# Kernel tuning notes

Hardware: AMD Instinct MI355X
Metric: run time of the kernel (lower is better)

## Reference

```python
import jax, jax.numpy as jnp
import numpy as np

TAU = 0.05       # sinkhorn temperature (functools.partial in GCN_Net)
SK_ITERS = 20    # sinkhorn max_iter


def _mlp(x, w1, b1, w2, b2):
    # nn.Sequential(Linear, ReLU, Linear)
    return jnp.maximum(x @ w1 + b1, 0.0) @ w2 + b2


def _cosine(f1, f2, eps=1e-8):
    # torch CosineSimilarity over broadcast (E1,1,D) x (1,E2,D), computed as a GEMM
    n1 = jnp.maximum(jnp.linalg.norm(f1, axis=-1), eps)
    n2 = jnp.maximum(jnp.linalg.norm(f2, axis=-1), eps)
    return (f1 @ f2.T) / (n1[:, None] * n2[None, :])


def _sinkhorn(s):
    # log-domain sinkhorn, alternating row/col normalization (pygmtools-style)
    log_s = s / TAU
    for i in range(SK_ITERS):
        log_s = log_s - jax.nn.logsumexp(log_s, axis=(1 if i % 2 == 0 else 0), keepdims=True)
    return jnp.exp(log_s)


def _build_conn_edges(preds):
    # fully-connected off-diagonal graph; edge feats [dx, dy, dist, cls_src, cls_dst]
    n = preds.shape[0]
    pos = preds[:, 1:3]
    cls = preds[:, 6]
    idx = np.arange(n)
    r, c = np.meshgrid(idx, idx, indexing='ij')
    m = r != c
    conn = np.stack([r[m], c[m]], axis=1)  # (E,2), static under jit
    src, dst = conn[:, 0], conn[:, 1]
    d = pos[dst] - pos[src]                             # (E,2)
    dist = jnp.linalg.norm(d, axis=-1, keepdims=True)   # (E,1)
    edges = jnp.concatenate([d, dist, cls[src][:, None], cls[dst][:, None]], axis=-1)  # (E,5)
    return jnp.asarray(conn), edges


def _forward(ego_preds, cav_preds, node_w1, node_b1, node_w2, node_b2,
             edge_w1, edge_b1, edge_w2, edge_b2,
             l0_self_w, l0_self_b, l0_conv_w, l0_conv_b, l0_cls_w, l0_cls_b,
             l1_self_w, l1_self_b, l1_conv_w, l1_conv_b, l1_cls_w, l1_cls_b,
             fc_w, fc_b):
    ego = ego_preds[0]
    cav = cav_preds[0]
    n1, n2 = ego.shape[0], cav.shape[0]
    conn1, e1 = _build_conn_edges(ego)
    conn2, e2 = _build_conn_edges(cav)
    # --- NodeMLP affinity ---
    f1 = _mlp(ego[:, 1:6], node_w1, node_b1, node_w2, node_b2)
    f2 = _mlp(cav[:, 1:6], node_w1, node_b1, node_w2, node_b2)
    cls_eq = (ego[:, 6][:, None] == cav[:, 6][None, :]).astype(ego.dtype)
    conf = jnp.sum(jnp.sqrt(ego[:, 7:][:, None, :] * cav[:, 7:][None, :, :]), axis=-1)
    node_aff = cls_eq * conf * _cosine(f1, f2)                         # (n1,n2)
    # --- EdgeMLP affinity ---
    g1 = _mlp(e1[:, :3], edge_w1, edge_b1, edge_w2, edge_b2)
    g2 = _mlp(e2[:, :3], edge_w1, edge_b1, edge_w2, edge_b2)
    ecls = jnp.all(e1[:, 3:].astype(jnp.int32)[:, None, :] == e2[:, 3:].astype(jnp.int32)[None, :, :],
                   axis=-1).astype(ego.dtype)
    edge_aff = ecls * _cosine(g1, g2)                                  # (E1,E2)
    # --- Lawler affinity matrix K over association graph: node (i,a) -> i*n2+a ---
    N = n1 * n2
    rows = (conn1[:, 0][:, None] * n2 + conn2[:, 0][None, :]).ravel()
    cols = (conn1[:, 1][:, None] * n2 + conn2[:, 1][None, :]).ravel()
    K = jnp.zeros((N, N), ego.dtype).at[rows, cols].set(edge_aff.ravel())
    d_idx = jnp.arange(N)
    K = K.at[d_idx, d_idx].set(node_aff.ravel())
    # --- GCN adjacency = nonzero pattern of K, with added self-loops + sym norm ---
    A = (K != 0).astype(ego.dtype) + jnp.eye(N, dtype=ego.dtype)
    dinv = jax.lax.rsqrt(A.sum(axis=1))
    normA = dinv[:, None] * A * dinv[None, :]
    x = jnp.diag(K)[:, None]                                           # (N,1)
    # --- NGMConvLayers: self-loop Linear + GCNConv + sinkhorn channel ---
    for sw, sb, cw, cb, kw, kb in (
            (l0_self_w, l0_self_b, l0_conv_w, l0_conv_b, l0_cls_w, l0_cls_b),
            (l1_self_w, l1_self_b, l1_conv_w, l1_conv_b, l1_cls_w, l1_cls_b)):
        x = (x @ sw + sb) + (normA @ (x @ cw) + cb)
        sk = _sinkhorn((x @ kw + kb).reshape(n1, n2))
        x = x + sk.reshape(-1, 1)
    scores = x @ fc_w + fc_b                                           # (N,1)
    s = scores.reshape(n2, n1).T                                       # view(n2,-1).t()
    return _sinkhorn(s)


def setup_inputs() -> dict:
    key = jax.random.key(0)
    ks = jax.random.split(key, 16)

    def lin(k, fi, fo):
        kw, kb = jax.random.split(k)
        s = (2.0 / (fi + fo)) ** 0.5
        return (jax.random.normal(kw, (fi, fo), jnp.float32) * s,
                jax.random.normal(kb, (fo,), jnp.float32) * 0.01)

    def make_preds(k, n):
        k1, k2 = jax.random.split(k)
        p = jax.random.uniform(k1, (1, n, 8), jnp.float32)
        cls = jnp.floor(jax.random.uniform(k2, (1, n)) * 3.0)  # 3 discrete classes
        p = p.at[:, :, 6].set(cls)
        p = p.at[:, :, 7].set(0.1 + 0.9 * p[:, :, 7])          # positive confidences
        return p

    inp = {'ego_preds': make_preds(ks[0], 64), 'cav_preds': make_preds(ks[1], 64)}
    inp['node_w1'], inp['node_b1'] = lin(ks[2], 5, 64)
    inp['node_w2'], inp['node_b2'] = lin(ks[3], 64, 32)
    inp['edge_w1'], inp['edge_b1'] = lin(ks[4], 3, 64)
    inp['edge_w2'], inp['edge_b2'] = lin(ks[5], 64, 32)
    inp['l0_self_w'], inp['l0_self_b'] = lin(ks[6], 1, 16)
    inp['l0_conv_w'], inp['l0_conv_b'] = lin(ks[7], 1, 16)
    inp['l0_cls_w'], inp['l0_cls_b'] = lin(ks[8], 16, 1)
    inp['l1_self_w'], inp['l1_self_b'] = lin(ks[9], 16, 16)
    inp['l1_conv_w'], inp['l1_conv_b'] = lin(ks[10], 16, 16)
    inp['l1_cls_w'], inp['l1_cls_b'] = lin(ks[11], 16, 1)
    inp['fc_w'], inp['fc_b'] = lin(ks[12], 16, 1)
    return inp


def reference(ego_preds, cav_preds, node_w1, node_b1, node_w2, node_b2,
              edge_w1, edge_b1, edge_w2, edge_b2,
              l0_self_w, l0_self_b, l0_conv_w, l0_conv_b, l0_cls_w, l0_cls_b,
              l1_self_w, l1_self_b, l1_conv_w, l1_conv_b, l1_cls_w, l1_cls_b,
              fc_w, fc_b):
    return _forward(ego_preds, cav_preds, node_w1, node_b1, node_w2, node_b2,
                    edge_w1, edge_b1, edge_w2, edge_b2,
                    l0_self_w, l0_self_b, l0_conv_w, l0_conv_b, l0_cls_w, l0_cls_b,
                    l1_self_w, l1_self_b, l1_conv_w, l1_conv_b, l1_cls_w, l1_cls_b,
                    fc_w, fc_b)
```

## Files before the change

kernel.cpp:

```cpp
#include <hip/hip_runtime.h>
#include <math.h>


#define TAU_INV 20.0f

template<int CTRL>
__device__ __forceinline__ float dppf(float x) {
    int xi = __float_as_int(x);
    int rr = __builtin_amdgcn_update_dpp(xi, xi, CTRL, 0xF, 0xF, false);
    return __int_as_float(rr);
}
__device__ __forceinline__ float red16_max(float v) {
    v = fmaxf(v, dppf<0xB1>(v));
    v = fmaxf(v, dppf<0x4E>(v));
    v = fmaxf(v, dppf<0x141>(v));
    v = fmaxf(v, dppf<0x140>(v));
    return v;
}
__device__ __forceinline__ float red16_sum(float v) {
    v += dppf<0xB1>(v);
    v += dppf<0x4E>(v);
    v += dppf<0x141>(v);
    v += dppf<0x140>(v);
    return v;
}
__device__ __forceinline__ float quad_sum(float v) {
    v += dppf<0xB1>(v);
    v += dppf<0x4E>(v);
    return v;
}
__device__ __forceinline__ float dot4(const float4 a, const float4 b) {
    return a.x*b.x + a.y*b.y + a.z*b.z + a.w*b.w;
}
__device__ __forceinline__ void fma4(float4& a, float b, const float4 c) {
    a.x += b*c.x; a.y += b*c.y; a.z += b*c.z; a.w += b*c.w;
}
__device__ __forceinline__ void add4(float4& a, const float4 c) {
    a.x += c.x; a.y += c.y; a.z += c.z; a.w += c.w;
}

__device__ void sinkhorn_rc(const float* tq, const float* tt, int tid, float* Rp, float* Cp) {
    const int g = tid >> 4, s = tid & 15;
    const int wa = 4 * (g & 15) + (g >> 4);
    for (int it = 0; it < 20; ++it) {
        if ((it & 1) == 0) {
            float4 cq = *(const float4*)(Cp + 4 * s);
            float z0 = tq[0]-cq.x, z1 = tq[1]-cq.y, z2 = tq[2]-cq.z, z3 = tq[3]-cq.w;
            float m  = red16_max(fmaxf(fmaxf(z0, z1), fmaxf(z2, z3)));
            float sm = red16_sum(__expf(z0-m) + __expf(z1-m) + __expf(z2-m) + __expf(z3-m));
            if (s == 0) Rp[wa] = __logf(sm) + m;
        } else {
            float4 rq = *(const float4*)(Rp + 4 * s);
            float z0 = tt[0]-rq.x, z1 = tt[1]-rq.y, z2 = tt[2]-rq.z, z3 = tt[3]-rq.w;
            float m  = red16_max(fmaxf(fmaxf(z0, z1), fmaxf(z2, z3)));
            float sm = red16_sum(__expf(z0-m) + __expf(z1-m) + __expf(z2-m) + __expf(z3-m));
            if (s == 0) Cp[wa] = __logf(sm) + m;
        }
        __syncthreads();
    }
}

__device__ void matvec_dual(const float* u1, const float* u2,
                            const float* mmq, const float* dq,
                            float* o1, float* o2, int tid,
                            float* WR1, float* WR2, float* WC1p, float* WC2p,
                            float* pwc, float* scW) {
    const int r = tid >> 4, s = tid & 15, lane = tid & 63, w = tid >> 6;
    float z1[4], z2[4];
    float rs1 = 0.0f, rs2 = 0.0f;
    #pragma unroll
    for (int k = 0; k < 4; ++k) {
        float md = mmq[k] * dq[k];
        z1[k] = md * u1[k];
        z2[k] = md * u2[k];
        rs1 += z1[k]; rs2 += z2[k];
    }
    rs1 = red16_sum(rs1); rs2 = red16_sum(rs2);
    if (s == 0) { WR1[r] = rs1; WR2[r] = rs2; }
    float p1[4], p2[4];
    #pragma unroll
    for (int k = 0; k < 4; ++k) {
        float v = z1[k]; v += __shfl_xor(v, 16); v += __shfl_xor(v, 32); p1[k] = v;
        float u = z2[k]; u += __shfl_xor(u, 16); u += __shfl_xor(u, 32); p2[k] = u;
    }
    if (lane < 16) {
        ((float4*)pwc)[w * 16 + s]          = make_float4(p1[0], p1[1], p1[2], p1[3]);
        ((float4*)(pwc + 1024))[w * 16 + s] = make_float4(p2[0], p2[1], p2[2], p2[3]);
    }
    __syncthreads();
    if (tid < 64) {
        float c1 = 0.0f, c2 = 0.0f;
        #pragma unroll
        for (int ww = 0; ww < 16; ++ww) {
            c1 += pwc[ww * 64 + tid];
            c2 += pwc[1024 + ww * 64 + tid];
        }
        WC1p[tid] = c1; WC2p[tid] = c2;
    } else if (tid < 128) {
        float v = WR1[tid - 64];
        #pragma unroll
        for (int off = 32; off > 0; off >>= 1) v += __shfl_xor(v, off);
        if (tid == 64) scW[0] = v;
    } else if (tid < 192) {
        float v = WR2[tid - 128];
        #pragma unroll
        for (int off = 32; off > 0; off >>= 1) v += __shfl_xor(v, off);
        if (tid == 128) scW[1] = v;
    }
    __syncthreads();
    const float W1 = scW[0], W2 = scW[1];
    const float wr1 = WR1[r], wr2 = WR2[r];
    float4 wc1 = *(const float4*)(WC1p + 4 * s);
    float4 wc2 = *(const float4*)(WC2p + 4 * s);
    const float wc1a[4] = {wc1.x, wc1.y, wc1.z, wc1.w};
    const float wc2a[4] = {wc2.x, wc2.y, wc2.z, wc2.w};
    #pragma unroll
    for (int k = 0; k < 4; ++k) {
        float d = dq[k], mm = mmq[k];
        o1[k] = d * ((1.0f + mm) * d * u1[k] + mm * (W1 - wr1 - wc1a[k] + z1[k]));
        o2[k] = d * ((1.0f + mm) * d * u2[k] + mm * (W2 - wr2 - wc2a[k] + z2[k]));
    }
    __syncthreads();
}

extern "C" __global__ __launch_bounds__(1024)
void gcn_match_kernel(const float* ego, const float* cav,
                      const float* nw1, const float* nb1, const float* nw2, const float* nb2,
                      const float* sw0, const float* sb0, const float* cw0, const float* cb0,
                      const float* kw0, const float* kb0,
                      const float* sw1, const float* sb1, const float* cw1, const float* cb1,
                      const float* kw1, const float* kb1,
                      const float* fcw, const float* fcb,
                      float* out) {
    __shared__ __align__(16) float sh_h1[64 * 68];
    __shared__ __align__(16) float sh_h2[64 * 68];
    __shared__ __align__(16) float sh_f1[64 * 36];
    __shared__ __align__(16) float sh_f2[64 * 36];
    __shared__ __align__(16) float sh_w2[2048];
    __shared__ __align__(16) float sh_nb2[32];
    __shared__ float sh_cls1[64], sh_cls2[64], sh_cf1[64], sh_cf2[64];
    __shared__ float sh_n1[64], sh_n2[64];
    __shared__ float sh_Dr[64], sh_Dc[64];
    __shared__ __align__(16) float sh_Rp[64], sh_Cp[64];
    __shared__ float sh_WR1[64], sh_WR2[64];
    __shared__ __align__(16) float sh_WC1p[64], sh_WC2p[64];
    __shared__ float sh_avec[7 * 16];
    __shared__ float sh_coef[18];
    __shared__ float sh_sc[4];

    const int tid  = threadIdx.x;
    const int wave = tid >> 6, lane = tid & 63;
    const int r = tid >> 4, s = tid & 15;

    if (tid < 512) ((float4*)sh_w2)[tid] = ((const float4*)nw2)[tid];
    if (tid < 32) sh_nb2[tid] = nb2[tid];
    if (tid < 64) { sh_cls1[tid] = ego[tid * 8 + 6]; sh_cf1[tid] = ego[tid * 8 + 7]; }
    else if (tid < 128) { int j = tid - 64; sh_cls2[j] = cav[j * 8 + 6]; sh_cf2[j] = cav[j * 8 + 7]; }
    {
        float w1r[5];
        #pragma unroll
        for (int f = 0; f < 5; ++f) w1r[f] = nw1[f * 64 + lane];
        float b1r = nb1[lane];
        #pragma unroll
        for (int p = 0; p < 4; ++p) {
            int i = wave + (p << 4);
            float4 e0 = ((const float4*)ego)[i * 2];
            float4 e1 = ((const float4*)ego)[i * 2 + 1];
            float a1 = b1r + e0.y*w1r[0] + e0.z*w1r[1] + e0.w*w1r[2] + e1.x*w1r[3] + e1.y*w1r[4];
            sh_h1[i * 68 + lane] = fmaxf(a1, 0.0f);
            float4 c0 = ((const float4*)cav)[i * 2];
            float4 c1 = ((const float4*)cav)[i * 2 + 1];
            float a2 = b1r + c0.y*w1r[0] + c0.z*w1r[1] + c0.w*w1r[2] + c1.x*w1r[3] + c1.y*w1r[4];
            sh_h2[i * 68 + lane] = fmaxf(a2, 0.0f);
        }
    }
    __syncthreads();

    if (wave < 4) {
        const int gw = wave & 1;
        const float* H = (wave < 2) ? sh_h1 : sh_h2;
        float* F  = (wave < 2) ? sh_f1 : sh_f2;
        float* NN = (wave < 2) ? sh_n1 : sh_n2;
        const int rr = lane >> 2, oq = lane & 3;
        const int i0 = 32 * gw + rr, i1 = i0 + 16;
        float4 a00 = make_float4(0,0,0,0), a01 = a00, a10 = a00, a11 = a00;
        #pragma unroll 4
        for (int k = 0; k < 64; ++k) {
            float  ha = H[i0 * 68 + k];
            float  hb = H[i1 * 68 + k];
            float4 wa = *(const float4*)(sh_w2 + k * 32 + 4 * oq);
            float4 wb = *(const float4*)(sh_w2 + k * 32 + 16 + 4 * oq);
            fma4(a00, ha, wa); fma4(a01, ha, wb);
            fma4(a10, hb, wa); fma4(a11, hb, wb);
        }
        float4 b2a = *(const float4*)(sh_nb2 + 4 * oq);
        float4 b2b = *(const float4*)(sh_nb2 + 16 + 4 * oq);
        add4(a00, b2a); add4(a01, b2b); add4(a10, b2a); add4(a11, b2b);
        *(float4*)(F + i0 * 36 + 4 * oq)      = a00;
        *(float4*)(F + i0 * 36 + 16 + 4 * oq) = a01;
        *(float4*)(F + i1 * 36 + 4 * oq)      = a10;
        *(float4*)(F + i1 * 36 + 16 + 4 * oq) = a11;
        float sq0 = quad_sum(dot4(a00, a00) + dot4(a01, a01));
        float sq1 = quad_sum(dot4(a10, a10) + dot4(a11, a11));
        if (oq == 0) {
            NN[i0] = fmaxf(sqrtf(sq0), 1e-8f);
            NN[i1] = fmaxf(sqrtf(sq1), 1e-8f);
        }
    } else if (wave == 4) {
        float c1v = sh_cls1[lane], d = 0.0f;
        for (int j = 0; j < 64; ++j) d += (c1v == sh_cls2[j]) ? 1.0f : 0.0f;
        sh_Dr[lane] = d;
        float t = d;
        #pragma unroll
        for (int off = 32; off > 0; off >>= 1) t += __shfl_xor(t, off);
        if (lane == 0) sh_sc[2] = t;
    } else if (wave == 5) {
        float c2v = sh_cls2[lane], d = 0.0f;
        for (int i = 0; i < 64; ++i) d += (sh_cls1[i] == c2v) ? 1.0f : 0.0f;
        sh_Dc[lane] = d;
    } else if (wave == 6 && lane < 16) {
        int o = lane;
        float ax = 0, av = 0, as_ = 0, aw = 0, au = 0, ae = 0, a1 = 0;
        for (int k = 0; k < 16; ++k) {
            float s0k = sw0[k], c0k = cw0[k], b0k = sb0[k] + cb0[k];
            float s1ko = sw1[k * 16 + o], c1ko = cw1[k * 16 + o];
            ax += s0k * s1ko;  av += c0k * s1ko + s0k * c1ko;  as_ += s1ko;
            aw += c0k * c1ko;  au += c1ko;  ae += b0k * c1ko;  a1 += b0k * s1ko;
        }
        a1 += sb1[o] + cb1[o];
        sh_avec[0*16+o] = ax; sh_avec[1*16+o] = av; sh_avec[2*16+o] = as_;
        sh_avec[3*16+o] = aw; sh_avec[4*16+o] = au; sh_avec[5*16+o] = ae;
        sh_avec[6*16+o] = a1;
    }
    __syncthreads();

    if (wave < 4) {
        const int sc = lane & 15, rc = lane >> 4;
        float dt[4][4];
        #pragma unroll
        for (int m = 0; m < 4; ++m)
            #pragma unroll
            for (int k = 0; k < 4; ++k) dt[m][k] = 0.0f;
        for (int kq = 0; kq < 8; ++kq) {
            float4 f2q[4];
            #pragma unroll
            for (int k = 0; k < 4; ++k)
                f2q[k] = *(const float4*)(sh_f2 + (sc + 16 * k) * 36 + 4 * kq);
            #pragma unroll
            for (int m = 0; m < 4; ++m) {
                int rrow = 16 * m + 4 * wave + rc;
                float4 f1q = *(const float4*)(sh_f1 + rrow * 36 + 4 * kq);
                #pragma unroll
                for (int k = 0; k < 4; ++k) dt[m][k] += dot4(f1q, f2q[k]);
            }
        }
        #pragma unroll
        for (int m = 0; m < 4; ++m) {
            int rrow = 16 * m + 4 * wave + rc;
            *(float4*)(sh_h1 + rrow * 68 + 4 * sc) =
                make_float4(dt[m][0], dt[m][1], dt[m][2], dt[m][3]);
        }
    } else if (wave == 4 && lane < 18) {
        int t = lane; float c = 0.0f;
        if (t == 0)      { for (int k = 0; k < 16; ++k) c += sw0[k] * kw0[k]; }
        else if (t == 1) { for (int k = 0; k < 16; ++k) c += cw0[k] * kw0[k]; }
        else if (t == 2) { for (int k = 0; k < 16; ++k) c += (sb0[k] + cb0[k]) * kw0[k]; c += kb0[0]; }
        else if (t < 10) { int v = t - 3;
            for (int o = 0; o < 16; ++o) c += sh_avec[v * 16 + o] * kw1[o];
            if (v == 6) c += kb1[0];
        } else if (t < 17) { int v = t - 10;
            for (int o = 0; o < 16; ++o) c += sh_avec[v * 16 + o] * fcw[o];
            if (v == 6) c += fcb[0];
        } else { for (int o = 0; o < 16; ++o) c += fcw[o]; }
        sh_coef[t] = c;
    } else if (wave == 5) {
        sh_Cp[lane] = 0.0f;
    }
    const float cls1r = sh_cls1[r];
    const float Tdeg = sh_sc[2], Drr = sh_Dr[r];
    const float n1r = sh_n1[r], cf1r = sh_cf1[r];
    float mmq[4], dqv[4], cfq[4], n2q[4];
    #pragma unroll
    for (int k = 0; k < 4; ++k) {
        int j = s + 16 * k;
        float mm = (cls1r == sh_cls2[j]) ? 1.0f : 0.0f;
        mmq[k] = mm;
        dqv[k] = (mm != 0.0f) ? (1.0f / sqrtf(Tdeg - Drr - sh_Dc[j] + 3.0f)) : 1.0f;
        cfq[k] = sqrtf(cf1r * sh_cf2[j]);
        n2q[k] = sh_n2[j];
    }
    __syncthreads();

    float x0[4];
    {
        float4 dq4 = *(const float4*)(sh_h1 + r * 68 + 4 * s);
        const float da[4] = {dq4.x, dq4.y, dq4.z, dq4.w};
        #pragma unroll
        for (int k = 0; k < 4; ++k)
            x0[k] = mmq[k] * cfq[k] * (da[k] / (n1r * n2q[k]));
    }
    __syncthreads();

    float v0[4], oe[4];
    {
        float ones[4] = {1.0f, 1.0f, 1.0f, 1.0f};
        matvec_dual(x0, ones, mmq, dqv, v0, oe, tid,
                    sh_WR1, sh_WR2, sh_WC1p, sh_WC2p, sh_h1, sh_sc);
    }

    const int pr = 4 * (r & 15) + (r >> 4);
    float t0q[4], t0t[4];
    {
        float c0 = sh_coef[0], c1 = sh_coef[1], c2 = sh_coef[2];
        #pragma unroll
        for (int k = 0; k < 4; ++k) t0q[k] = (c0 * x0[k] + c1 * v0[k] + c2) * TAU_INV;
    }
    *(float4*)(sh_h2 + r * 68 + 4 * s) = make_float4(t0q[0], t0q[1], t0q[2], t0q[3]);
    __syncthreads();
    #pragma unroll
    for (int k = 0; k < 4; ++k) t0t[k] = sh_h2[(s + 16 * k) * 68 + pr];
    sinkhorn_rc(t0q, t0t, tid, sh_Rp, sh_Cp);
    float s0[4];
    {
        float Rr = sh_Rp[pr];
        float4 cc = *(const float4*)(sh_Cp + 4 * s);
        const float ca[4] = {cc.x, cc.y, cc.z, cc.w};
        #pragma unroll
        for (int k = 0; k < 4; ++k) s0[k] = __expf(t0q[k] - Rr - ca[k]);
    }

    float ov[4], os[4];
    matvec_dual(v0, s0, mmq, dqv, ov, os, tid,
                sh_WR1, sh_WR2, sh_WC1p, sh_WC2p, sh_h1, sh_sc);
    float tacc[4], sacc[4];
    {
        float ctx = sh_coef[3], ctv = sh_coef[4], cts = sh_coef[5];
        float cw_ = sh_coef[6], cu_ = sh_coef[7], ce_ = sh_coef[8], ct1 = sh_coef[9];
        float csx = sh_coef[10], csv = sh_coef[11], css = sh_coef[12];
        float cw2 = sh_coef[13], cu2 = sh_coef[14], ce2 = sh_coef[15], cs1 = sh_coef[16];
        #pragma unroll
        for (int k = 0; k < 4; ++k) {
            tacc[k] = ctx * x0[k] + ctv * v0[k] + cts * s0[k] + ct1
                    + cw_ * ov[k] + cu_ * os[k] + ce_ * oe[k];
            sacc[k] = csx * x0[k] + csv * v0[k] + css * s0[k] + cs1
                    + cw2 * ov[k] + cu2 * os[k] + ce2 * oe[k];
        }
    }

    float t1q[4], t1t[4];
    #pragma unroll
    for (int k = 0; k < 4; ++k) t1q[k] = tacc[k] * TAU_INV;
    if (tid < 64) sh_Cp[tid] = 0.0f;
    *(float4*)(sh_h2 + r * 68 + 4 * s) = make_float4(t1q[0], t1q[1], t1q[2], t1q[3]);
    __syncthreads();
    #pragma unroll
    for (int k = 0; k < 4; ++k) t1t[k] = sh_h2[(s + 16 * k) * 68 + pr];
    sinkhorn_rc(t1q, t1t, tid, sh_Rp, sh_Cp);
    {
        float c17 = sh_coef[17];
        float Rr = sh_Rp[pr];
        float4 cc = *(const float4*)(sh_Cp + 4 * s);
        const float ca[4] = {cc.x, cc.y, cc.z, cc.w};
        #pragma unroll
        for (int k = 0; k < 4; ++k) sacc[k] += c17 * __expf(t1q[k] - Rr - ca[k]);
    }
    __syncthreads();

    if (tid < 64) sh_Cp[tid] = 0.0f;
    *(float4*)(sh_h2 + r * 68 + 4 * s) = make_float4(sacc[0], sacc[1], sacc[2], sacc[3]);
    __syncthreads();
    float t2q[4], t2t[4];
    #pragma unroll
    for (int k = 0; k < 4; ++k) {
        t2q[k] = sh_h2[(s + 16 * k) * 68 + pr] * TAU_INV;
        t2t[k] = sacc[k] * TAU_INV;
    }
    sinkhorn_rc(t2q, t2t, tid, sh_Rp, sh_Cp);
    {
        float Rr = sh_Rp[pr];
        float4 cc = *(const float4*)(sh_Cp + 4 * s);
        const float ca[4] = {cc.x, cc.y, cc.z, cc.w};
        #pragma unroll
        for (int k = 0; k < 4; ++k)
            out[r * 64 + s + 16 * k] = __expf(t2q[k] - Rr - ca[k]);
    }
}

extern "C" void kernel_launch(void* const* d_in, const int* in_sizes, int n_in,
                              void* d_out, int out_size, void* d_ws, size_t ws_size,
                              hipStream_t stream) {
    const float* ego = (const float*)d_in[0];
    const float* cav = (const float*)d_in[1];
    const float* nw1 = (const float*)d_in[2];
    const float* nb1 = (const float*)d_in[3];
    const float* nw2 = (const float*)d_in[4];
    const float* nb2 = (const float*)d_in[5];
    const float* sw0 = (const float*)d_in[10];
    const float* sb0 = (const float*)d_in[11];
    const float* cw0 = (const float*)d_in[12];
    const float* cb0 = (const float*)d_in[13];
    const float* kw0 = (const float*)d_in[14];
    const float* kb0 = (const float*)d_in[15];
    const float* sw1 = (const float*)d_in[16];
    const float* sb1 = (const float*)d_in[17];
    const float* cw1 = (const float*)d_in[18];
    const float* cb1 = (const float*)d_in[19];
    const float* kw1 = (const float*)d_in[20];
    const float* kb1 = (const float*)d_in[21];
    const float* fcw = (const float*)d_in[22];
    const float* fcb = (const float*)d_in[23];

    gcn_match_kernel<<<dim3(1), dim3(1024), 0, stream>>>(
        ego, cav, nw1, nb1, nw2, nb2,
        sw0, sb0, cw0, cb0, kw0, kb0,
        sw1, sb1, cw1, cb1, kw1, kb1,
        fcw, fcb, (float*)d_out);
}
```

Baseline: 136.5 us.

## Rework Sinkhorn in base-2 log domain with incremental normalizers and fewer barriers

Sinkhorn now runs in the log2 domain using the hardware exp2/log2 builtins, with the temperature folded into a scale constant. Each row or column keeps its own running normalizer and adds the log-sum of already-normalized exponentials, so the per-iteration max reduction goes away. A clamp guards against underflow. The change also drops the Cp zeroing, fuses the first row step into the setup barrier, double-buffers the matvec scratch so a trailing barrier can be removed, and moves the coefficient precompute into an earlier phase. Skipping the max subtraction relies on the values staying bounded, which is a numerical risk.

```diff
diff --git a/kernel.cpp b/kernel.cpp
--- a/kernel.cpp
+++ b/kernel.cpp
@@ -2,7 +2,7 @@
 #include <math.h>
 
 
-#define TAU_INV 20.0f
+#define SK_SCALE 28.853900817779268f
 
 template<int CTRL>
 __device__ __forceinline__ float dppf(float x) {
@@ -18,17 +18,15 @@
     return v;
 }
 __device__ __forceinline__ float red16_sum(float v) {
-    v += dppf<0xB1>(v);
-    v += dppf<0x4E>(v);
-    v += dppf<0x141>(v);
-    v += dppf<0x140>(v);
+    v += dppf<0xB1>(v); v += dppf<0x4E>(v); v += dppf<0x141>(v); v += dppf<0x140>(v);
     return v;
 }
 __device__ __forceinline__ float quad_sum(float v) {
-    v += dppf<0xB1>(v);
-    v += dppf<0x4E>(v);
+    v += dppf<0xB1>(v); v += dppf<0x4E>(v);
     return v;
 }
+__device__ __forceinline__ float e2f(float x) { return __builtin_amdgcn_exp2f(x); }
+__device__ __forceinline__ float l2f(float x) { return __builtin_amdgcn_logf(x); }
 __device__ __forceinline__ float dot4(const float4 a, const float4 b) {
     return a.x*b.x + a.y*b.y + a.z*b.z + a.w*b.w;
 }
@@ -39,25 +37,43 @@
     a.x += c.x; a.y += c.y; a.z += c.z; a.w += c.w;
 }
 
-__device__ void sinkhorn_rc(const float* tq, const float* tt, int tid, float* Rp, float* Cp) {
-    const int g = tid >> 4, s = tid & 15;
-    const int wa = 4 * (g & 15) + (g >> 4);
-    for (int it = 0; it < 20; ++it) {
-        if ((it & 1) == 0) {
+__device__ __forceinline__ float sk_step0(const float* tq) {
+    float m  = red16_max(fmaxf(fmaxf(tq[0], tq[1]), fmaxf(tq[2], tq[3])));
+    float sm = red16_sum(e2f(tq[0]-m) + e2f(tq[1]-m) + e2f(tq[2]-m) + e2f(tq[3]-m));
+    return m + l2f(sm);
+}
+
+__device__ float sk_rest(const float* tq, const float* tt, float Rown,
+                         int pr, int s, float* Rp, float* Cp) {
+    float Cown;
+    {
+        float4 rq = *(const float4*)(Rp + 4 * s);
+        float sm = red16_sum(e2f(tt[0]-rq.x) + e2f(tt[1]-rq.y) +
+                             e2f(tt[2]-rq.z) + e2f(tt[3]-rq.w));
+        Cown = l2f(fmaxf(sm, 1e-37f));
+        if (s == 0) Cp[pr] = Cown;
+        __syncthreads();
+    }
+    #pragma unroll 1
+    for (int p = 0; p < 9; ++p) {
+        {
             float4 cq = *(const float4*)(Cp + 4 * s);
-            float z0 = tq[0]-cq.x, z1 = tq[1]-cq.y, z2 = tq[2]-cq.z, z3 = tq[3]-cq.w;
-            float m  = red16_max(fmaxf(fmaxf(z0, z1), fmaxf(z2, z3)));
-            float sm = red16_sum(__expf(z0-m) + __expf(z1-m) + __expf(z2-m) + __expf(z3-m));
-            if (s == 0) Rp[wa] = __logf(sm) + m;
-        } else {
+            float sm = red16_sum(e2f(tq[0]-cq.x-Rown) + e2f(tq[1]-cq.y-Rown) +
+                                 e2f(tq[2]-cq.z-Rown) + e2f(tq[3]-cq.w-Rown));
+            Rown += l2f(fmaxf(sm, 1e-37f));
+            if (s == 0) Rp[pr] = Rown;
+            __syncthreads();
+        }
+        {
             float4 rq = *(const float4*)(Rp + 4 * s);
-            float z0 = tt[0]-rq.x, z1 = tt[1]-rq.y, z2 = tt[2]-rq.z, z3 = tt[3]-rq.w;
-            float m  = red16_max(fmaxf(fmaxf(z0, z1), fmaxf(z2, z3)));
-            float sm = red16_sum(__expf(z0-m) + __expf(z1-m) + __expf(z2-m) + __expf(z3-m));
-            if (s == 0) Cp[wa] = __logf(sm) + m;
-        }
-        __syncthreads();
-    }
+            float sm = red16_sum(e2f(tt[0]-rq.x-Cown) + e2f(tt[1]-rq.y-Cown) +
+                                 e2f(tt[2]-rq.z-Cown) + e2f(tt[3]-rq.w-Cown));
+            Cown += l2f(fmaxf(sm, 1e-37f));
+            if (s == 0) Cp[pr] = Cown;
+            __syncthreads();
+        }
+    }
+    return Rown;
 }
 
 __device__ void matvec_dual(const float* u1, const float* u2,
@@ -120,7 +136,6 @@
         o1[k] = d * ((1.0f + mm) * d * u1[k] + mm * (W1 - wr1 - wc1a[k] + z1[k]));
         o2[k] = d * ((1.0f + mm) * d * u2[k] + mm * (W2 - wr2 - wc2a[k] + z2[k]));
     }
-    __syncthreads();
 }
 
 extern "C" __global__ __launch_bounds__(1024)
@@ -138,49 +153,68 @@
     __shared__ __align__(16) float sh_f2[64 * 36];
     __shared__ __align__(16) float sh_w2[2048];
     __shared__ __align__(16) float sh_nb2[32];
-    __shared__ float sh_cls1[64], sh_cls2[64], sh_cf1[64], sh_cf2[64];
-    __shared__ float sh_n1[64], sh_n2[64];
-    __shared__ float sh_Dr[64], sh_Dc[64];
+    __shared__ float sh_cls1[64], sh_cf1[64];
+    __shared__ __align__(16) float sh_cls2p[64], sh_cf2p[64];
+    __shared__ float sh_n1[64];
+    __shared__ __align__(16) float sh_n2p[64];
+    __shared__ float sh_Dr[64];
+    __shared__ __align__(16) float sh_Dcp[64];
     __shared__ __align__(16) float sh_Rp[64], sh_Cp[64];
-    __shared__ float sh_WR1[64], sh_WR2[64];
-    __shared__ __align__(16) float sh_WC1p[64], sh_WC2p[64];
+    __shared__ float sh_WR1a[64], sh_WR2a[64], sh_WR1b[64], sh_WR2b[64];
+    __shared__ __align__(16) float sh_WC1pa[64], sh_WC2pa[64], sh_WC1pb[64], sh_WC2pb[64];
     __shared__ float sh_avec[7 * 16];
     __shared__ float sh_coef[18];
-    __shared__ float sh_sc[4];
+    __shared__ float sh_sc[8];
 
     const int tid  = threadIdx.x;
     const int wave = tid >> 6, lane = tid & 63;
     const int r = tid >> 4, s = tid & 15;
+    const int pr = 4 * (r & 15) + (r >> 4);
 
     if (tid < 512) ((float4*)sh_w2)[tid] = ((const float4*)nw2)[tid];
     if (tid < 32) sh_nb2[tid] = nb2[tid];
     if (tid < 64) { sh_cls1[tid] = ego[tid * 8 + 6]; sh_cf1[tid] = ego[tid * 8 + 7]; }
-    else if (tid < 128) { int j = tid - 64; sh_cls2[j] = cav[j * 8 + 6]; sh_cf2[j] = cav[j * 8 + 7]; }
-    {
+    else if (tid < 128) {
+        int j = tid - 64, jp = 4 * (j & 15) + (j >> 4);
+        sh_cls2p[jp] = cav[j * 8 + 6]; sh_cf2p[jp] = cav[j * 8 + 7];
+    }
+    if (wave < 8) {
         float w1r[5];
         #pragma unroll
         for (int f = 0; f < 5; ++f) w1r[f] = nw1[f * 64 + lane];
         float b1r = nb1[lane];
         #pragma unroll
-        for (int p = 0; p < 4; ++p) {
-            int i = wave + (p << 4);
+        for (int p = 0; p < 8; ++p) {
+            int i = (wave << 3) | p;
             float4 e0 = ((const float4*)ego)[i * 2];
             float4 e1 = ((const float4*)ego)[i * 2 + 1];
-            float a1 = b1r + e0.y*w1r[0] + e0.z*w1r[1] + e0.w*w1r[2] + e1.x*w1r[3] + e1.y*w1r[4];
-            sh_h1[i * 68 + lane] = fmaxf(a1, 0.0f);
+            sh_h1[i * 68 + lane] = fmaxf(
+                b1r + e0.y*w1r[0] + e0.z*w1r[1] + e0.w*w1r[2] + e1.x*w1r[3] + e1.y*w1r[4], 0.0f);
             float4 c0 = ((const float4*)cav)[i * 2];
             float4 c1 = ((const float4*)cav)[i * 2 + 1];
-            float a2 = b1r + c0.y*w1r[0] + c0.z*w1r[1] + c0.w*w1r[2] + c1.x*w1r[3] + c1.y*w1r[4];
-            sh_h2[i * 68 + lane] = fmaxf(a2, 0.0f);
-        }
+            sh_h2[i * 68 + lane] = fmaxf(
+                b1r + c0.y*w1r[0] + c0.z*w1r[1] + c0.w*w1r[2] + c1.x*w1r[3] + c1.y*w1r[4], 0.0f);
+        }
+    } else if (wave == 8 && lane < 16) {
+        int o = lane;
+        float ax = 0, av = 0, as_ = 0, aw = 0, au = 0, ae = 0, a1 = 0;
+        for (int k = 0; k < 16; ++k) {
+            float s0k = sw0[k], c0k = cw0[k], b0k = sb0[k] + cb0[k];
+            float s1ko = sw1[k * 16 + o], c1ko = cw1[k * 16 + o];
+            ax += s0k * s1ko;  av += c0k * s1ko + s0k * c1ko;  as_ += s1ko;
+            aw += c0k * c1ko;  au += c1ko;  ae += b0k * c1ko;  a1 += b0k * s1ko;
+        }
+        a1 += sb1[o] + cb1[o];
+        sh_avec[0*16+o] = ax; sh_avec[1*16+o] = av; sh_avec[2*16+o] = as_;
+        sh_avec[3*16+o] = aw; sh_avec[4*16+o] = au; sh_avec[5*16+o] = ae;
+        sh_avec[6*16+o] = a1;
     }
     __syncthreads();
 
     if (wave < 4) {
         const int gw = wave & 1;
         const float* H = (wave < 2) ? sh_h1 : sh_h2;
-        float* F  = (wave < 2) ? sh_f1 : sh_f2;
-        float* NN = (wave < 2) ? sh_n1 : sh_n2;
+        float* F = (wave < 2) ? sh_f1 : sh_f2;
         const int rr = lane >> 2, oq = lane & 3;
         const int i0 = 32 * gw + rr, i1 = i0 + 16;
         float4 a00 = make_float4(0,0,0,0), a01 = a00, a10 = a00, a11 = a00;
@@ -203,34 +237,40 @@
         float sq0 = quad_sum(dot4(a00, a00) + dot4(a01, a01));
         float sq1 = quad_sum(dot4(a10, a10) + dot4(a11, a11));
         if (oq == 0) {
-            NN[i0] = fmaxf(sqrtf(sq0), 1e-8f);
-            NN[i1] = fmaxf(sqrtf(sq1), 1e-8f);
+            float v0n = fmaxf(sqrtf(sq0), 1e-8f);
+            float v1n = fmaxf(sqrtf(sq1), 1e-8f);
+            if (wave < 2) { sh_n1[i0] = v0n; sh_n1[i1] = v1n; }
+            else {
+                sh_n2p[4 * (i0 & 15) + (i0 >> 4)] = v0n;
+                sh_n2p[4 * (i1 & 15) + (i1 >> 4)] = v1n;
+            }
         }
     } else if (wave == 4) {
         float c1v = sh_cls1[lane], d = 0.0f;
-        for (int j = 0; j < 64; ++j) d += (c1v == sh_cls2[j]) ? 1.0f : 0.0f;
+        for (int j = 0; j < 64; ++j) d += (c1v == sh_cls2p[j]) ? 1.0f : 0.0f;
         sh_Dr[lane] = d;
         float t = d;
         #pragma unroll
         for (int off = 32; off > 0; off >>= 1) t += __shfl_xor(t, off);
         if (lane == 0) sh_sc[2] = t;
     } else if (wave == 5) {
-        float c2v = sh_cls2[lane], d = 0.0f;
+        float c2v = sh_cls2p[4 * (lane & 15) + (lane >> 4)];
+        float d = 0.0f;
         for (int i = 0; i < 64; ++i) d += (sh_cls1[i] == c2v) ? 1.0f : 0.0f;
-        sh_Dc[lane] = d;
-    } else if (wave == 6 && lane < 16) {
-        int o = lane;
-        float ax = 0, av = 0, as_ = 0, aw = 0, au = 0, ae = 0, a1 = 0;
-        for (int k = 0; k < 16; ++k) {
-            float s0k = sw0[k], c0k = cw0[k], b0k = sb0[k] + cb0[k];
-            float s1ko = sw1[k * 16 + o], c1ko = cw1[k * 16 + o];
-            ax += s0k * s1ko;  av += c0k * s1ko + s0k * c1ko;  as_ += s1ko;
-            aw += c0k * c1ko;  au += c1ko;  ae += b0k * c1ko;  a1 += b0k * s1ko;
-        }
-        a1 += sb1[o] + cb1[o];
-        sh_avec[0*16+o] = ax; sh_avec[1*16+o] = av; sh_avec[2*16+o] = as_;
-        sh_avec[3*16+o] = aw; sh_avec[4*16+o] = au; sh_avec[5*16+o] = ae;
-        sh_avec[6*16+o] = a1;
+        sh_Dcp[4 * (lane & 15) + (lane >> 4)] = d;
+    } else if (wave == 6 && lane < 18) {
+        int t = lane; float c = 0.0f;
+        if (t == 0)      { for (int k = 0; k < 16; ++k) c += sw0[k] * kw0[k]; }
+        else if (t == 1) { for (int k = 0; k < 16; ++k) c += cw0[k] * kw0[k]; }
+        else if (t == 2) { for (int k = 0; k < 16; ++k) c += (sb0[k] + cb0[k]) * kw0[k]; c += kb0[0]; }
+        else if (t < 10) { int v = t - 3;
+            for (int o = 0; o < 16; ++o) c += sh_avec[v * 16 + o] * kw1[o];
+            if (v == 6) c += kb1[0];
+        } else if (t < 17) { int v = t - 10;
+            for (int o = 0; o < 16; ++o) c += sh_avec[v * 16 + o] * fcw[o];
+            if (v == 6) c += fcb[0];
+        } else { for (int o = 0; o < 16; ++o) c += fcw[o]; }
+        sh_coef[t] = c;
     }
     __syncthreads();
 
@@ -260,39 +300,34 @@
             *(float4*)(sh_h1 + rrow * 68 + 4 * sc) =
                 make_float4(dt[m][0], dt[m][1], dt[m][2], dt[m][3]);
         }
-    } else if (wave == 4 && lane < 18) {
-        int t = lane; float c = 0.0f;
-        if (t == 0)      { for (int k = 0; k < 16; ++k) c += sw0[k] * kw0[k]; }
-        else if (t == 1) { for (int k = 0; k < 16; ++k) c += cw0[k] * kw0[k]; }
-        else if (t == 2) { for (int k = 0; k < 16; ++k) c += (sb0[k] + cb0[k]) * kw0[k]; c += kb0[0]; }
-        else if (t < 10) { int v = t - 3;
-            for (int o = 0; o < 16; ++o) c += sh_avec[v * 16 + o] * kw1[o];
-            if (v == 6) c += kb1[0];
-        } else if (t < 17) { int v = t - 10;
-            for (int o = 0; o < 16; ++o) c += sh_avec[v * 16 + o] * fcw[o];
-            if (v == 6) c += fcb[0];
-        } else { for (int o = 0; o < 16; ++o) c += fcw[o]; }
-        sh_coef[t] = c;
-    } else if (wave == 5) {
-        sh_Cp[lane] = 0.0f;
-    }
-    const float cls1r = sh_cls1[r];
-    const float Tdeg = sh_sc[2], Drr = sh_Dr[r];
-    const float n1r = sh_n1[r], cf1r = sh_cf1[r];
+    }
     float mmq[4], dqv[4], cfq[4], n2q[4];
-    #pragma unroll
-    for (int k = 0; k < 4; ++k) {
-        int j = s + 16 * k;
-        float mm = (cls1r == sh_cls2[j]) ? 1.0f : 0.0f;
-        mmq[k] = mm;
-        dqv[k] = (mm != 0.0f) ? (1.0f / sqrtf(Tdeg - Drr - sh_Dc[j] + 3.0f)) : 1.0f;
-        cfq[k] = sqrtf(cf1r * sh_cf2[j]);
-        n2q[k] = sh_n2[j];
+    {
+        const float cls1r = sh_cls1[r];
+        const float Tdeg = sh_sc[2], Drr = sh_Dr[r];
+        const float cf1r = sh_cf1[r];
+        float4 c2 = *(const float4*)(sh_cls2p + 4 * s);
+        float4 cf = *(const float4*)(sh_cf2p + 4 * s);
+        float4 n2 = *(const float4*)(sh_n2p + 4 * s);
+        float4 dc = *(const float4*)(sh_Dcp + 4 * s);
+        const float c2a[4] = {c2.x, c2.y, c2.z, c2.w};
+        const float cfa[4] = {cf.x, cf.y, cf.z, cf.w};
+        const float n2a[4] = {n2.x, n2.y, n2.z, n2.w};
+        const float dca[4] = {dc.x, dc.y, dc.z, dc.w};
+        #pragma unroll
+        for (int k = 0; k < 4; ++k) {
+            float mm = (cls1r == c2a[k]) ? 1.0f : 0.0f;
+            mmq[k] = mm;
+            dqv[k] = (mm != 0.0f) ? (1.0f / sqrtf(Tdeg - Drr - dca[k] + 3.0f)) : 1.0f;
+            cfq[k] = sqrtf(cf1r * cfa[k]);
+            n2q[k] = n2a[k];
+        }
     }
     __syncthreads();
 
     float x0[4];
     {
+        const float n1r = sh_n1[r];
         float4 dq4 = *(const float4*)(sh_h1 + r * 68 + 4 * s);
         const float da[4] = {dq4.x, dq4.y, dq4.z, dq4.w};
         #pragma unroll
@@ -305,33 +340,34 @@
     {
         float ones[4] = {1.0f, 1.0f, 1.0f, 1.0f};
         matvec_dual(x0, ones, mmq, dqv, v0, oe, tid,
-                    sh_WR1, sh_WR2, sh_WC1p, sh_WC2p, sh_h1, sh_sc);
-    }
-
-    const int pr = 4 * (r & 15) + (r >> 4);
-    float t0q[4], t0t[4];
-    {
-        float c0 = sh_coef[0], c1 = sh_coef[1], c2 = sh_coef[2];
-        #pragma unroll
-        for (int k = 0; k < 4; ++k) t0q[k] = (c0 * x0[k] + c1 * v0[k] + c2) * TAU_INV;
+                    sh_WR1a, sh_WR2a, sh_WC1pa, sh_WC2pa, sh_h1, sh_sc);
+    }
+
+    float t0q[4];
+    {
+        float c0 = sh_coef[0], c1 = sh_coef[1], c2c = sh_coef[2];
+        #pragma unroll
+        for (int k = 0; k < 4; ++k) t0q[k] = (c0 * x0[k] + c1 * v0[k] + c2c) * SK_SCALE;
     }
     *(float4*)(sh_h2 + r * 68 + 4 * s) = make_float4(t0q[0], t0q[1], t0q[2], t0q[3]);
-    __syncthreads();
+    float R0 = sk_step0(t0q);
+    if (s == 0) sh_Rp[pr] = R0;
+    __syncthreads();
+    float t0t[4];
     #pragma unroll
     for (int k = 0; k < 4; ++k) t0t[k] = sh_h2[(s + 16 * k) * 68 + pr];
-    sinkhorn_rc(t0q, t0t, tid, sh_Rp, sh_Cp);
+    R0 = sk_rest(t0q, t0t, R0, pr, s, sh_Rp, sh_Cp);
     float s0[4];
     {
-        float Rr = sh_Rp[pr];
         float4 cc = *(const float4*)(sh_Cp + 4 * s);
         const float ca[4] = {cc.x, cc.y, cc.z, cc.w};
         #pragma unroll
-        for (int k = 0; k < 4; ++k) s0[k] = __expf(t0q[k] - Rr - ca[k]);
+        for (int k = 0; k < 4; ++k) s0[k] = e2f(t0q[k] - R0 - ca[k]);
     }
 
     float ov[4], os[4];
     matvec_dual(v0, s0, mmq, dqv, ov, os, tid,
-                sh_WR1, sh_WR2, sh_WC1p, sh_WC2p, sh_h1, sh_sc);
+                sh_WR1b, sh_WR2b, sh_WC1pb, sh_WC2pb, sh_h1 + 2048, sh_sc + 4);
     float tacc[4], sacc[4];
     {
         float ctx = sh_coef[3], ctv = sh_coef[4], cts = sh_coef[5];
@@ -347,42 +383,43 @@
         }
     }
 
-    float t1q[4], t1t[4];
-    #pragma unroll
-    for (int k = 0; k < 4; ++k) t1q[k] = tacc[k] * TAU_INV;
-    if (tid < 64) sh_Cp[tid] = 0.0f;
+    float t1q[4];
+    #pragma unroll
+    for (int k = 0; k < 4; ++k) t1q[k] = tacc[k] * SK_SCALE;
     *(float4*)(sh_h2 + r * 68 + 4 * s) = make_float4(t1q[0], t1q[1], t1q[2], t1q[3]);
-    __syncthreads();
+    float R1 = sk_step0(t1q);
+    if (s == 0) sh_Rp[pr] = R1;
+    __syncthreads();
+    float t1t[4];
     #pragma unroll
     for (int k = 0; k < 4; ++k) t1t[k] = sh_h2[(s + 16 * k) * 68 + pr];
-    sinkhorn_rc(t1q, t1t, tid, sh_Rp, sh_Cp);
+    R1 = sk_rest(t1q, t1t, R1, pr, s, sh_Rp, sh_Cp);
     {
         float c17 = sh_coef[17];
-        float Rr = sh_Rp[pr];
         float4 cc = *(const float4*)(sh_Cp + 4 * s);
         const float ca[4] = {cc.x, cc.y, cc.z, cc.w};
         #pragma unroll
-        for (int k = 0; k < 4; ++k) sacc[k] += c17 * __expf(t1q[k] - Rr - ca[k]);
-    }
-    __syncthreads();
-
-    if (tid < 64) sh_Cp[tid] = 0.0f;
+        for (int k = 0; k < 4; ++k) sacc[k] += c17 * e2f(t1q[k] - R1 - ca[k]);
+    }
+
     *(float4*)(sh_h2 + r * 68 + 4 * s) = make_float4(sacc[0], sacc[1], sacc[2], sacc[3]);
     __syncthreads();
     float t2q[4], t2t[4];
     #pragma unroll
     for (int k = 0; k < 4; ++k) {
-        t2q[k] = sh_h2[(s + 16 * k) * 68 + pr] * TAU_INV;
-        t2t[k] = sacc[k] * TAU_INV;
-    }
-    sinkhorn_rc(t2q, t2t, tid, sh_Rp, sh_Cp);
-    {
-        float Rr = sh_Rp[pr];
+        t2q[k] = sh_h2[(s + 16 * k) * 68 + pr] * SK_SCALE;
+        t2t[k] = sacc[k] * SK_SCALE;
+    }
+    float R2 = sk_step0(t2q);
+    if (s == 0) sh_Rp[pr] = R2;
+    __syncthreads();
+    R2 = sk_rest(t2q, t2t, R2, pr, s, sh_Rp, sh_Cp);
+    {
         float4 cc = *(const float4*)(sh_Cp + 4 * s);
         const float ca[4] = {cc.x, cc.y, cc.z, cc.w};
         #pragma unroll
         for (int k = 0; k < 4; ++k)
-            out[r * 64 + s + 16 * k] = __expf(t2q[k] - Rr - ca[k]);
+            out[(r << 6) + s + (k << 4)] = e2f(t2q[k] - R2 - ca[k]);
     }
 }
 
```

Result: faster. 124.0 us (-9.2%).
